# Optimization experiments

Measured on AMD Instinct MI355X. Metric: run time of the kernel, lower is better.

Reference implementation:

```python
import jax, jax.numpy as jnp
import numpy as np

B, K, HH, WW = 512, 256, 16, 16   # batch, channels (K//2 of init K=512), latent H, W
KH = 128                          # GRU hidden size
F = 16                            # future_window_lin


def gru_forward(seq, h0, W_ih, W_hh, b_ih, b_hh):
    # seq: (B,T,K) batch_first, h0: (B,KH). PyTorch GRU gate order: r, z, n.
    gx = jnp.einsum('btk,gk->btg', seq, W_ih) + b_ih  # (B,T,3*KH)

    def step(h, gx_t):
        gh = h @ W_hh.T + b_hh
        xr, xz, xn = jnp.split(gx_t, 3, axis=-1)
        hr, hz, hn = jnp.split(gh, 3, axis=-1)
        r = jax.nn.sigmoid(xr + hr)
        z = jax.nn.sigmoid(xz + hz)
        n = jnp.tanh(xn + r * hn)
        h_new = (1.0 - z) * n + z * h
        return h_new, h_new

    hT, outs = jax.lax.scan(step, h0, jnp.swapaxes(gx, 0, 1))  # outs: (T,B,KH)
    return jnp.swapaxes(outs, 0, 1), hT


def setup_inputs() -> dict:
    key = jax.random.key(0)
    ks = jax.random.split(key, 9)
    s = 0.05
    return {
        'z_q_x_st': jax.random.normal(ks[0], (B, K, HH, WW), jnp.float32),
        'z_e_x': jax.random.normal(ks[1], (B, K, HH, WW), jnp.float32),
        'z_q_x': jax.random.normal(ks[2], (B, K, HH, WW), jnp.float32),
        'hidden': jnp.zeros((1, B, KH), jnp.float32),
        'W_ih': jax.random.normal(ks[3], (3 * KH, K), jnp.float32) * s,
        'W_hh': jax.random.normal(ks[4], (3 * KH, KH), jnp.float32) * s,
        'b_ih': jnp.zeros((3 * KH,), jnp.float32),
        'b_hh': jnp.zeros((3 * KH,), jnp.float32),
        'Wk_w': jax.random.normal(ks[5], (F, K, KH), jnp.float32) * s,
        'Wk_b': jnp.zeros((F, K), jnp.float32),
        'p_sample': 100,
    }


def reference(z_q_x_st, z_e_x, z_q_x, hidden, W_ih, W_hh, b_ih, b_hh, Wk_w, Wk_b, p_sample):
    batch, k, h, w = z_e_x.shape
    f = Wk_w.shape[0]
    # (B,K,H,W) -> (B,H*W,K); row = idx//W, col = idx%W is just the row-major flat index
    z_flat = jnp.transpose(z_q_x_st, (0, 2, 3, 1)).reshape(batch, h * w, k)
    # encoded samples at flat positions p_sample+1 .. p_sample+F  -> (F,B,K)
    encoded = jnp.swapaxes(z_flat[:, p_sample + 1: p_sample + 1 + f, :], 0, 1)
    # GRU over the causal prefix; c_t = output at step p_sample (the last one)
    seq = z_flat[:, : p_sample + 1, :]
    out, _ = gru_forward(seq, hidden[0], W_ih, W_hh, b_ih, b_hh)
    c_t = out[:, -1, :]  # (B,KH)
    # per-step linear heads, batched: (F,B,K)
    pred = jnp.einsum('fkh,bh->fbk', Wk_w, c_t) + Wk_b[:, None, :]
    # totals[i] = encoded[i] @ pred[i].T  -> (F,B,B)
    totals = jnp.einsum('fbk,fck->fbc', encoded, pred)
    lsm = jax.nn.log_softmax(totals, axis=2)
    diag_sum = jnp.sum(jnp.diagonal(lsm, axis1=1, axis2=2))
    nce = -diag_sum / (batch * f)
    # 'correct' only reflects the last loop iteration in the torch code
    last = totals[-1]
    sm = jax.nn.softmax(last, axis=1)       # softmax over dim=1, then argmax over dim=0
    preds_idx = jnp.argmax(sm, axis=0)
    correct = jnp.sum(preds_idx == jnp.arange(batch))
    accuracy = correct.astype(jnp.float32) / batch
    return accuracy, nce, z_e_x, z_q_x
```

## Files before the change

kernel.cpp:

```cpp
#include <hip/hip_runtime.h>
#include <math.h>

#define NB_B   512
#define NK     256
#define NKH    128
#define NG3    384
#define NT     101
#define NF     16
#define NPASS  (512ull*256*256)

#define OFF_GX   0ull
#define N_GX     (512ull*101*384)
#define OFF_CT   (OFF_GX + N_GX)
#define OFF_ENC  (OFF_CT + 512ull*128)
#define OFF_PRED (OFF_ENC + 16ull*512*256)
#define OFF_TOT  (OFF_PRED + 16ull*512*256)
#define OFF_LSE  (OFF_TOT + 16ull*512*512)
#define OFF_DML  (OFF_LSE + 8192ull)
#define OFF_WT   (OFF_DML + 8192ull)
#define OFF_WKT  (OFF_WT + 384ull*256)
#define OFF_CNT  (OFF_WKT + 16ull*128*256)

__global__ __launch_bounds__(256) void k_transpose(
    const float* __restrict__ W_ih, const float* __restrict__ Wk_w,
    float* __restrict__ Wt, float* __restrict__ Wkt, int* __restrict__ cnt) {
  int idx = blockIdx.x * 256 + threadIdx.x;
  if (idx == 0) *cnt = 0;
  if (idx < 384 * 256) {
    int g = idx % 384, k = idx / 384;
    Wt[idx] = W_ih[g * 256 + k];
  }
  if (idx < 16 * 128 * 256) {
    int k = idx & 255, h = (idx >> 8) & 127, f = idx >> 15;
    Wkt[idx] = Wk_w[(f * 256 + k) * 128 + h];
  }
}

__global__ __launch_bounds__(768) void k_gx(
    const float* __restrict__ zq, const float* __restrict__ Wt,
    const float* __restrict__ b_ih, const float* __restrict__ b_hh,
    float* __restrict__ gx) {
  __shared__ float Xs[32][104];
  __shared__ float Ws[32 * 384];
  int b = blockIdx.x;
  int tid = threadIdx.x;
  int q = tid % 96;
  int tt = tid / 96;
  int g0 = q * 4;
  int t0 = tt * 13;
  int lane = tid & 63, wid = tid >> 6;
  float acc[4][13];
#pragma unroll
  for (int i = 0; i < 4; i++)
#pragma unroll
    for (int j = 0; j < 13; j++) acc[i][j] = 0.f;
  const float* zb = zq + (size_t)b * 65536;
  for (int kc = 0; kc < 8; kc++) {
    __syncthreads();
    for (int k = wid; k < 32; k += 12) {
      int kk = kc * 32 + k;
      Xs[k][lane] = zb[kk * 256 + lane];
      int t1 = 64 + lane;
      if (t1 < 104) Xs[k][t1] = (t1 < 101) ? zb[kk * 256 + t1] : 0.f;
    }
    {
      const float4* wsrc = (const float4*)(Wt + (size_t)kc * 32 * 384);
      float4* wdst = (float4*)Ws;
      for (int i = tid; i < 3072; i += 768) wdst[i] = wsrc[i];
    }
    __syncthreads();
    for (int k = 0; k < 32; k++) {
      float4 w = *(const float4*)&Ws[k * 384 + g0];
      const float* xr = &Xs[k][t0];
#pragma unroll
      for (int j = 0; j < 13; j++) {
        float x = xr[j];
        acc[0][j] += w.x * x;
        acc[1][j] += w.y * x;
        acc[2][j] += w.z * x;
        acc[3][j] += w.w * x;
      }
    }
  }
  float4 bias = *(const float4*)&b_ih[g0];
  if (g0 + 3 < 256) {
    bias.x += b_hh[g0 + 0]; bias.y += b_hh[g0 + 1];
    bias.z += b_hh[g0 + 2]; bias.w += b_hh[g0 + 3];
  }
#pragma unroll
  for (int j = 0; j < 13; j++) {
    int t = t0 + j;
    if (t < 101) {
      float4 v = make_float4(acc[0][j] + bias.x, acc[1][j] + bias.y,
                             acc[2][j] + bias.z, acc[3][j] + bias.w);
      *(float4*)&gx[(size_t)t * (512 * 384) + b * 384 + g0] = v;
    }
  }
}

__global__ __launch_bounds__(1024, 4) void k_scan(
    const float* __restrict__ gx, const float* __restrict__ W_hh,
    const float* __restrict__ b_hh, const float* __restrict__ hidden,
    float* __restrict__ ct,
    const float* __restrict__ src0, const float* __restrict__ src1,
    float2* __restrict__ d0, float2* __restrict__ d1) {
  __shared__ float hs[2][128];
  __shared__ float ghp[2][2][384];
  int tid = threadIdx.x;
  int b0 = blockIdx.x * 2;
  bool copy_role = (tid >= 768);

  int kh = tid / 384;
  int g = tid % 384;
  int lane = tid & 63;
  float w[64];
  float cxr = 0.f, cxz = 0.f, cxn = 0.f, nxr = 0.f, nxz = 0.f, nxn = 0.f;
  float bhn = 0.f;
  const float2* S0 = (const float2*)src0;
  const float2* S1 = (const float2*)src1;
  int c = tid - 768;
  size_t sbase = (size_t)blockIdx.x * 65536;
  int p = 0;

  if (!copy_role) {
    const float* wp = W_hh + g * 128 + kh * 64;
#pragma unroll
    for (int i = 0; i < 16; i++) {
      float4 v = *(const float4*)(wp + 4 * i);
      w[4 * i + 0] = v.x; w[4 * i + 1] = v.y;
      w[4 * i + 2] = v.z; w[4 * i + 3] = v.w;
    }
    if (tid < 256) {
      int r = tid >> 7, k = tid & 127;
      hs[r][k] = hidden[(b0 + r) * 128 + k];
      bhn = b_hh[256 + k];
      const float* gxb = gx + (b0 + r) * 384;
      cxr = gxb[k]; cxz = gxb[128 + k]; cxn = gxb[256 + k];
    }
  }
  __syncthreads();

  for (int t = 0; t < 101; t++) {
    if (!copy_role) {
      float hr0 = hs[0][kh * 64 + lane];
      float hr1 = hs[1][kh * 64 + lane];
      float a0 = 0.f, a1 = 0.f;
#pragma unroll
      for (int j = 0; j < 64; j++) {
        float h0 = __int_as_float(__builtin_amdgcn_readlane(__float_as_int(hr0), j));
        float h1 = __int_as_float(__builtin_amdgcn_readlane(__float_as_int(hr1), j));
        a0 = fmaf(w[j], h0, a0);
        a1 = fmaf(w[j], h1, a1);
      }
      ghp[0][kh][g] = a0;
      ghp[1][kh][g] = a1;
      if (tid < 256 && t < 100) {
        int r = tid >> 7, k = tid & 127;
        const float* gxb = gx + (size_t)(t + 1) * (512 * 384) + (b0 + r) * 384;
        nxr = gxb[k]; nxz = gxb[128 + k]; nxn = gxb[256 + k];
      }
    } else {
#pragma unroll
      for (int uu = 0; uu < 5; uu++) {
        int u = p + uu;
        size_t idx = sbase + (size_t)(u >> 1) * 256 + c;
        if (u & 1) d1[idx] = S1[idx];
        else       d0[idx] = S0[idx];
      }
      p += 5;
    }
    __syncthreads();
    if (!copy_role && tid < 256) {
      int r = tid >> 7, k = tid & 127;
      float hrr = ghp[r][0][k] + ghp[r][1][k];
      float hzz = ghp[r][0][128 + k] + ghp[r][1][128 + k];
      float hnn = ghp[r][0][256 + k] + ghp[r][1][256 + k] + bhn;
      float rr = 1.f / (1.f + __expf(-(cxr + hrr)));
      float zz = 1.f / (1.f + __expf(-(cxz + hzz)));
      float nn = tanhf(cxn + rr * hnn);
      hs[r][k] = (1.f - zz) * nn + zz * hs[r][k];
      cxr = nxr; cxz = nxz; cxn = nxn;
    }
    __syncthreads();
  }

  if (!copy_role && tid < 256) {
    int r = tid >> 7, k = tid & 127;
    ct[(b0 + r) * 128 + k] = hs[r][k];
  }
  if (copy_role) {
    for (; p < 512; p++) {
      size_t idx = sbase + (size_t)(p >> 1) * 256 + c;
      if (p & 1) d1[idx] = S1[idx];
      else       d0[idx] = S0[idx];
    }
  }
}

__global__ __launch_bounds__(256) void k_enc(const float* __restrict__ zq,
                                             float* __restrict__ enc) {
  __shared__ float tile[256][17];
  int b = blockIdx.x, tid = threadIdx.x;
  const float* zb = zq + (size_t)b * 65536;
  for (int pass = 0; pass < 16; pass++) {
    int idx = pass * 256 + tid;
    int k = idx >> 4, f = idx & 15;
    tile[k][f] = zb[k * 256 + 101 + f];
  }
  __syncthreads();
  for (int f = 0; f < 16; f++)
    enc[(size_t)f * 131072 + b * 256 + tid] = tile[tid][f];
}

__global__ __launch_bounds__(256) void k_pred(
    const float* __restrict__ Wkt, const float* __restrict__ Wk_b,
    const float* __restrict__ ct, float* __restrict__ pred) {
  __shared__ float cts[32][128];
  int f = blockIdx.x, c0 = blockIdx.y * 32;
  int tid = threadIdx.x;
  for (int pass = 0; pass < 16; pass++) {
    int idx = pass * 256 + tid;
    int cc = idx >> 7, h = idx & 127;
    cts[cc][h] = ct[(c0 + cc) * 128 + h];
  }
  __syncthreads();
  float acc[32];
#pragma unroll
  for (int i = 0; i < 32; i++) acc[i] = 0.f;
  const float* wb = Wkt + (size_t)f * 32768 + tid;
  for (int h = 0; h < 128; h += 4) {
    float w0 = wb[(h + 0) * 256], w1 = wb[(h + 1) * 256];
    float w2 = wb[(h + 2) * 256], w3 = wb[(h + 3) * 256];
#pragma unroll
    for (int cc = 0; cc < 32; cc++) {
      float4 cv = *(const float4*)&cts[cc][h];
      acc[cc] += w0 * cv.x + w1 * cv.y + w2 * cv.z + w3 * cv.w;
    }
  }
  float bias = Wk_b[f * 256 + tid];
#pragma unroll
  for (int cc = 0; cc < 32; cc++)
    pred[((size_t)f * 512 + c0 + cc) * 256 + tid] = acc[cc] + bias;
}

__global__ __launch_bounds__(256) void k_totals(
    const float* __restrict__ enc, const float* __restrict__ pred,
    float* __restrict__ tot) {
  __shared__ float As[32][68];
  __shared__ float Bs[32][68];
  int f = blockIdx.z, b0 = blockIdx.y * 64, c0 = blockIdx.x * 64;
  int tid = threadIdx.x;
  int tx = tid & 15, ty = tid >> 4;
  float acc[4][4];
#pragma unroll
  for (int i = 0; i < 4; i++)
#pragma unroll
    for (int j = 0; j < 4; j++) acc[i][j] = 0.f;
  const float* Ab = enc + (size_t)f * 131072;
  const float* Bb = pred + (size_t)f * 131072;
  int lr = tid >> 3;
  int lc = (tid & 7) * 4;
  for (int kc = 0; kc < 8; kc++) {
    int k0 = kc * 32;
    __syncthreads();
    float4 av0 = *(const float4*)&Ab[(b0 + lr) * 256 + k0 + lc];
    float4 av1 = *(const float4*)&Ab[(b0 + 32 + lr) * 256 + k0 + lc];
    float4 bv0 = *(const float4*)&Bb[(c0 + lr) * 256 + k0 + lc];
    float4 bv1 = *(const float4*)&Bb[(c0 + 32 + lr) * 256 + k0 + lc];
    As[lc + 0][lr] = av0.x; As[lc + 1][lr] = av0.y;
    As[lc + 2][lr] = av0.z; As[lc + 3][lr] = av0.w;
    As[lc + 0][lr + 32] = av1.x; As[lc + 1][lr + 32] = av1.y;
    As[lc + 2][lr + 32] = av1.z; As[lc + 3][lr + 32] = av1.w;
    Bs[lc + 0][lr] = bv0.x; Bs[lc + 1][lr] = bv0.y;
    Bs[lc + 2][lr] = bv0.z; Bs[lc + 3][lr] = bv0.w;
    Bs[lc + 0][lr + 32] = bv1.x; Bs[lc + 1][lr + 32] = bv1.y;
    Bs[lc + 2][lr + 32] = bv1.z; Bs[lc + 3][lr + 32] = bv1.w;
    __syncthreads();
#pragma unroll
    for (int kk = 0; kk < 32; kk++) {
      float4 a = *(const float4*)&As[kk][ty * 4];
      float4 bq = *(const float4*)&Bs[kk][tx * 4];
      acc[0][0] += a.x * bq.x; acc[0][1] += a.x * bq.y;
      acc[0][2] += a.x * bq.z; acc[0][3] += a.x * bq.w;
      acc[1][0] += a.y * bq.x; acc[1][1] += a.y * bq.y;
      acc[1][2] += a.y * bq.z; acc[1][3] += a.y * bq.w;
      acc[2][0] += a.z * bq.x; acc[2][1] += a.z * bq.y;
      acc[2][2] += a.z * bq.z; acc[2][3] += a.z * bq.w;
      acc[3][0] += a.w * bq.x; acc[3][1] += a.w * bq.y;
      acc[3][2] += a.w * bq.z; acc[3][3] += a.w * bq.w;
    }
  }
#pragma unroll
  for (int i = 0; i < 4; i++) {
    float4 v = make_float4(acc[i][0], acc[i][1], acc[i][2], acc[i][3]);
    *(float4*)&tot[(size_t)f * 262144 + (b0 + ty * 4 + i) * 512 + c0 + tx * 4] = v;
  }
}

__global__ __launch_bounds__(64) void k_lse(const float* __restrict__ tot,
                                            float* __restrict__ lse,
                                            float* __restrict__ dml) {
  int row = blockIdx.x;
  int b = row & 511;
  int lane = threadIdx.x;
  const float* tr = tot + (size_t)row * 512;
  float v[8];
  float mx = -1e30f;
#pragma unroll
  for (int i = 0; i < 8; i++) { v[i] = tr[i * 64 + lane]; mx = fmaxf(mx, v[i]); }
#pragma unroll
  for (int s = 32; s > 0; s >>= 1) mx = fmaxf(mx, __shfl_xor(mx, s));
  float sum = 0.f;
#pragma unroll
  for (int i = 0; i < 8; i++) sum += __expf(v[i] - mx);
#pragma unroll
  for (int s = 32; s > 0; s >>= 1) sum += __shfl_xor(sum, s);
  if (lane == 0) {
    float l = __logf(sum) + mx;
    lse[row] = l;
    dml[row] = tr[b] - l;
  }
}

__global__ __launch_bounds__(64) void k_acc(const float* __restrict__ tot,
                                            const float* __restrict__ lse,
                                            int* __restrict__ cnt) {
  int c = blockIdx.x;
  int lane = threadIdx.x;
  const float* t15 = tot + (size_t)15 * 262144;
  const float* l15 = lse + 15 * 512;
  float best = -1e30f;
  int bi = 1 << 30;
  for (int b = lane; b < 512; b += 64) {
    float v = t15[(size_t)b * 512 + c] - l15[b];
    if (v > best) { best = v; bi = b; }
  }
  for (int s = 32; s > 0; s >>= 1) {
    float ov = __shfl_xor(best, s);
    int oi = __shfl_xor(bi, s);
    if (ov > best || (ov == best && oi < bi)) { best = ov; bi = oi; }
  }
  if (lane == 0 && bi == c) atomicAdd(cnt, 1);
}

__global__ __launch_bounds__(256) void k_fin(const float* __restrict__ dml,
                                             const int* __restrict__ cnt,
                                             float* __restrict__ out) {
  __shared__ float red[256];
  int tid = threadIdx.x;
  float s = 0.f;
  for (int i = tid; i < 8192; i += 256) s += dml[i];
  red[tid] = s;
  __syncthreads();
  for (int st = 128; st > 0; st >>= 1) {
    if (tid < st) red[tid] += red[tid + st];
    __syncthreads();
  }
  if (tid == 0) {
    out[1] = -red[0] / 8192.f;
    out[0] = (float)(*cnt) / 512.f;
  }
}

extern "C" void kernel_launch(void* const* d_in, const int* in_sizes, int n_in,
                              void* d_out, int out_size, void* d_ws, size_t ws_size,
                              hipStream_t stream) {
  const float* zq   = (const float*)d_in[0];
  const float* ze   = (const float*)d_in[1];
  const float* zqx  = (const float*)d_in[2];
  const float* hid  = (const float*)d_in[3];
  const float* W_ih = (const float*)d_in[4];
  const float* W_hh = (const float*)d_in[5];
  const float* b_ih = (const float*)d_in[6];
  const float* b_hh = (const float*)d_in[7];
  const float* Wk_w = (const float*)d_in[8];
  const float* Wk_b = (const float*)d_in[9];
  float* out = (float*)d_out;
  float* ws  = (float*)d_ws;

  k_transpose<<<2048, 256, 0, stream>>>(W_ih, Wk_w, ws + OFF_WT, ws + OFF_WKT,
                                        (int*)(ws + OFF_CNT));
  k_gx<<<512, 768, 0, stream>>>(zq, ws + OFF_WT, b_ih, b_hh, ws + OFF_GX);
  k_scan<<<256, 1024, 0, stream>>>(ws + OFF_GX, W_hh, b_hh, hid, ws + OFF_CT,
                                   ze, zqx,
                                   (float2*)(out + 2), (float2*)(out + 2 + NPASS));
  k_enc<<<512, 256, 0, stream>>>(zq, ws + OFF_ENC);
  k_pred<<<dim3(16, 16), 256, 0, stream>>>(ws + OFF_WKT, Wk_b, ws + OFF_CT, ws + OFF_PRED);
  k_totals<<<dim3(8, 8, 16), 256, 0, stream>>>(ws + OFF_ENC, ws + OFF_PRED, ws + OFF_TOT);
  k_lse<<<8192, 64, 0, stream>>>(ws + OFF_TOT, ws + OFF_LSE, ws + OFF_DML);
  k_acc<<<512, 64, 0, stream>>>(ws + OFF_TOT, ws + OFF_LSE, (int*)(ws + OFF_CNT));
  k_fin<<<1, 256, 0, stream>>>(ws + OFF_DML, (const int*)(ws + OFF_CNT), out);
}
```

Before: 912.5 us.

## Widen gx GEMM register tile and pin scan W_hh weights in vector registers

The gx projection kernel now runs 384 threads per block, and each thread computes 8 gates by 13 timesteps instead of 4 by 13. This doubles register-level reuse of each shared-memory X load and halves the thread count. In the GRU scan, the 64 recurrent weights per thread are held as 16 float4 vectors, and an empty asm barrier at each step forces them to stay resident in VGPRs rather than be spilled or reloaded. The dot product is written out by hand with readlane broadcasts. The risks are higher register pressure in k_gx and constrained compiler scheduling in the scan.

```diff
diff --git a/kernel.cpp b/kernel.cpp
--- a/kernel.cpp
+++ b/kernel.cpp
@@ -21,6 +21,8 @@
 #define OFF_WKT  (OFF_WT + 384ull*256)
 #define OFF_CNT  (OFF_WKT + 16ull*128*256)
 
+typedef float f4v __attribute__((ext_vector_type(4)));
+
 __global__ __launch_bounds__(256) void k_transpose(
     const float* __restrict__ W_ih, const float* __restrict__ Wk_w,
     float* __restrict__ Wt, float* __restrict__ Wkt, int* __restrict__ cnt) {
@@ -36,7 +38,7 @@
   }
 }
 
-__global__ __launch_bounds__(768) void k_gx(
+__global__ __launch_bounds__(384, 2) void k_gx(
     const float* __restrict__ zq, const float* __restrict__ Wt,
     const float* __restrict__ b_ih, const float* __restrict__ b_hh,
     float* __restrict__ gx) {
@@ -44,20 +46,20 @@
   __shared__ float Ws[32 * 384];
   int b = blockIdx.x;
   int tid = threadIdx.x;
-  int q = tid % 96;
-  int tt = tid / 96;
-  int g0 = q * 4;
+  int q = tid % 48;
+  int tt = tid / 48;
+  int g0 = q * 8;
   int t0 = tt * 13;
   int lane = tid & 63, wid = tid >> 6;
-  float acc[4][13];
-#pragma unroll
-  for (int i = 0; i < 4; i++)
+  float acc[8][13];
+#pragma unroll
+  for (int i = 0; i < 8; i++)
 #pragma unroll
     for (int j = 0; j < 13; j++) acc[i][j] = 0.f;
   const float* zb = zq + (size_t)b * 65536;
   for (int kc = 0; kc < 8; kc++) {
     __syncthreads();
-    for (int k = wid; k < 32; k += 12) {
+    for (int k = wid; k < 32; k += 6) {
       int kk = kc * 32 + k;
       Xs[k][lane] = zb[kk * 256 + lane];
       int t1 = 64 + lane;
@@ -66,37 +68,60 @@
     {
       const float4* wsrc = (const float4*)(Wt + (size_t)kc * 32 * 384);
       float4* wdst = (float4*)Ws;
-      for (int i = tid; i < 3072; i += 768) wdst[i] = wsrc[i];
+      for (int i = tid; i < 3072; i += 384) wdst[i] = wsrc[i];
     }
     __syncthreads();
     for (int k = 0; k < 32; k++) {
-      float4 w = *(const float4*)&Ws[k * 384 + g0];
+      float4 wa = *(const float4*)&Ws[k * 384 + g0];
+      float4 wb = *(const float4*)&Ws[k * 384 + g0 + 4];
       const float* xr = &Xs[k][t0];
 #pragma unroll
       for (int j = 0; j < 13; j++) {
         float x = xr[j];
-        acc[0][j] += w.x * x;
-        acc[1][j] += w.y * x;
-        acc[2][j] += w.z * x;
-        acc[3][j] += w.w * x;
+        acc[0][j] += wa.x * x;
+        acc[1][j] += wa.y * x;
+        acc[2][j] += wa.z * x;
+        acc[3][j] += wa.w * x;
+        acc[4][j] += wb.x * x;
+        acc[5][j] += wb.y * x;
+        acc[6][j] += wb.z * x;
+        acc[7][j] += wb.w * x;
       }
     }
   }
-  float4 bias = *(const float4*)&b_ih[g0];
-  if (g0 + 3 < 256) {
-    bias.x += b_hh[g0 + 0]; bias.y += b_hh[g0 + 1];
-    bias.z += b_hh[g0 + 2]; bias.w += b_hh[g0 + 3];
+  float4 ba = *(const float4*)&b_ih[g0];
+  float4 bb = *(const float4*)&b_ih[g0 + 4];
+  if (g0 < 256) {
+    ba.x += b_hh[g0 + 0]; ba.y += b_hh[g0 + 1];
+    ba.z += b_hh[g0 + 2]; ba.w += b_hh[g0 + 3];
+    bb.x += b_hh[g0 + 4]; bb.y += b_hh[g0 + 5];
+    bb.z += b_hh[g0 + 6]; bb.w += b_hh[g0 + 7];
   }
 #pragma unroll
   for (int j = 0; j < 13; j++) {
     int t = t0 + j;
     if (t < 101) {
-      float4 v = make_float4(acc[0][j] + bias.x, acc[1][j] + bias.y,
-                             acc[2][j] + bias.z, acc[3][j] + bias.w);
-      *(float4*)&gx[(size_t)t * (512 * 384) + b * 384 + g0] = v;
-    }
-  }
-}
+      float* gp = &gx[(size_t)t * (512 * 384) + b * 384 + g0];
+      *(float4*)gp = make_float4(acc[0][j] + ba.x, acc[1][j] + ba.y,
+                                 acc[2][j] + ba.z, acc[3][j] + ba.w);
+      *(float4*)(gp + 4) = make_float4(acc[4][j] + bb.x, acc[5][j] + bb.y,
+                                       acc[6][j] + bb.z, acc[7][j] + bb.w);
+    }
+  }
+}
+
+#define RL(x, J) __int_as_float(__builtin_amdgcn_readlane(__float_as_int(x), (J)))
+#define DOT4(W, J)                                                   \
+  do {                                                               \
+    a0 = fmaf(W.x, RL(hr0, (J) + 0), a0);                            \
+    a1 = fmaf(W.x, RL(hr1, (J) + 0), a1);                            \
+    a0 = fmaf(W.y, RL(hr0, (J) + 1), a0);                            \
+    a1 = fmaf(W.y, RL(hr1, (J) + 1), a1);                            \
+    a0 = fmaf(W.z, RL(hr0, (J) + 2), a0);                            \
+    a1 = fmaf(W.z, RL(hr1, (J) + 2), a1);                            \
+    a0 = fmaf(W.w, RL(hr0, (J) + 3), a0);                            \
+    a1 = fmaf(W.w, RL(hr1, (J) + 3), a1);                            \
+  } while (0)
 
 __global__ __launch_bounds__(1024, 4) void k_scan(
     const float* __restrict__ gx, const float* __restrict__ W_hh,
@@ -113,7 +138,7 @@
   int kh = tid / 384;
   int g = tid % 384;
   int lane = tid & 63;
-  float w[64];
+  f4v w0, w1, w2, w3, w4, w5, w6, w7, w8, w9, wA, wB, wC, wD, wE, wF;
   float cxr = 0.f, cxz = 0.f, cxn = 0.f, nxr = 0.f, nxz = 0.f, nxn = 0.f;
   float bhn = 0.f;
   const float2* S0 = (const float2*)src0;
@@ -123,13 +148,11 @@
   int p = 0;
 
   if (!copy_role) {
-    const float* wp = W_hh + g * 128 + kh * 64;
-#pragma unroll
-    for (int i = 0; i < 16; i++) {
-      float4 v = *(const float4*)(wp + 4 * i);
-      w[4 * i + 0] = v.x; w[4 * i + 1] = v.y;
-      w[4 * i + 2] = v.z; w[4 * i + 3] = v.w;
-    }
+    const f4v* wp = (const f4v*)(W_hh + g * 128 + kh * 64);
+    w0 = wp[0];  w1 = wp[1];  w2 = wp[2];  w3 = wp[3];
+    w4 = wp[4];  w5 = wp[5];  w6 = wp[6];  w7 = wp[7];
+    w8 = wp[8];  w9 = wp[9];  wA = wp[10]; wB = wp[11];
+    wC = wp[12]; wD = wp[13]; wE = wp[14]; wF = wp[15];
     if (tid < 256) {
       int r = tid >> 7, k = tid & 127;
       hs[r][k] = hidden[(b0 + r) * 128 + k];
@@ -142,16 +165,17 @@
 
   for (int t = 0; t < 101; t++) {
     if (!copy_role) {
+      asm volatile("" : "+v"(w0), "+v"(w1), "+v"(w2), "+v"(w3),
+                        "+v"(w4), "+v"(w5), "+v"(w6), "+v"(w7),
+                        "+v"(w8), "+v"(w9), "+v"(wA), "+v"(wB),
+                        "+v"(wC), "+v"(wD), "+v"(wE), "+v"(wF));
       float hr0 = hs[0][kh * 64 + lane];
       float hr1 = hs[1][kh * 64 + lane];
       float a0 = 0.f, a1 = 0.f;
-#pragma unroll
-      for (int j = 0; j < 64; j++) {
-        float h0 = __int_as_float(__builtin_amdgcn_readlane(__float_as_int(hr0), j));
-        float h1 = __int_as_float(__builtin_amdgcn_readlane(__float_as_int(hr1), j));
-        a0 = fmaf(w[j], h0, a0);
-        a1 = fmaf(w[j], h1, a1);
-      }
+      DOT4(w0, 0);  DOT4(w1, 4);  DOT4(w2, 8);  DOT4(w3, 12);
+      DOT4(w4, 16); DOT4(w5, 20); DOT4(w6, 24); DOT4(w7, 28);
+      DOT4(w8, 32); DOT4(w9, 36); DOT4(wA, 40); DOT4(wB, 44);
+      DOT4(wC, 48); DOT4(wD, 52); DOT4(wE, 56); DOT4(wF, 60);
       ghp[0][kh][g] = a0;
       ghp[1][kh][g] = a1;
       if (tid < 256 && t < 100) {
@@ -380,7 +404,7 @@
 
   k_transpose<<<2048, 256, 0, stream>>>(W_ih, Wk_w, ws + OFF_WT, ws + OFF_WKT,
                                         (int*)(ws + OFF_CNT));
-  k_gx<<<512, 768, 0, stream>>>(zq, ws + OFF_WT, b_ih, b_hh, ws + OFF_GX);
+  k_gx<<<512, 384, 0, stream>>>(zq, ws + OFF_WT, b_ih, b_hh, ws + OFF_GX);
   k_scan<<<256, 1024, 0, stream>>>(ws + OFF_GX, W_hh, b_hh, hid, ws + OFF_CT,
                                    ze, zqx,
                                    (float2*)(out + 2), (float2*)(out + 2 + NPASS));
```

New measurement: 962.5 us. 5.5% more time.

## Broadcast GRU hidden state via global memory and scalar loads instead of readlane

Applied to the files above, without the earlier changes.

The recurrent scan no longer keeps the hidden state in shared memory and broadcasts it with per-lane readlane calls. Each step's hidden state is now written to a global history buffer, which reuses the encoder/pred workspace region. The matvec threads then read it back with s_load_dwordx16 scalar loads in four chunks, which removes the 128 readlane instructions per step. The cost is a global-memory round trip and four serialized scalar-load waits on the critical path of every step. It also relies on vector stores becoming visible to scalar loads after the barrier.

```diff
diff --git a/kernel.cpp b/kernel.cpp
--- a/kernel.cpp
+++ b/kernel.cpp
@@ -20,6 +20,10 @@
 #define OFF_WT   (OFF_DML + 8192ull)
 #define OFF_WKT  (OFF_WT + 384ull*256)
 #define OFF_CNT  (OFF_WKT + 16ull*128*256)
+#define OFF_HG   OFF_ENC
+
+typedef float f4v __attribute__((ext_vector_type(4)));
+typedef int  si16 __attribute__((ext_vector_type(16)));
 
 __global__ __launch_bounds__(256) void k_transpose(
     const float* __restrict__ W_ih, const float* __restrict__ Wk_w,
@@ -98,41 +102,55 @@
   }
 }
 
+#define SCHUNK(C, OFF0, OFF1)                                            \
+  {                                                                      \
+    si16 ha_, hb_;                                                       \
+    asm volatile("s_load_dwordx16 %0, %2, " OFF0 "\n\t"                  \
+                 "s_load_dwordx16 %1, %2, " OFF1 "\n\t"                  \
+                 "s_waitcnt lgkmcnt(0)"                                  \
+                 : "=s"(ha_), "=s"(hb_)                                  \
+                 : "s"(ua)                                               \
+                 : "memory");                                            \
+    _Pragma("unroll")                                                    \
+    for (int jj = 0; jj < 16; jj++) {                                    \
+      float wv = wq[(C) * 4 + (jj >> 2)][jj & 3];                        \
+      a0 = fmaf(wv, __int_as_float(ha_[jj]), a0);                        \
+      a1 = fmaf(wv, __int_as_float(hb_[jj]), a1);                        \
+    }                                                                    \
+  }
+
 __global__ __launch_bounds__(1024, 4) void k_scan(
     const float* __restrict__ gx, const float* __restrict__ W_hh,
     const float* __restrict__ b_hh, const float* __restrict__ hidden,
     float* __restrict__ ct,
     const float* __restrict__ src0, const float* __restrict__ src1,
-    float2* __restrict__ d0, float2* __restrict__ d1) {
-  __shared__ float hs[2][128];
+    float2* __restrict__ d0, float2* __restrict__ d1,
+    float* __restrict__ hgl) {
   __shared__ float ghp[2][2][384];
   int tid = threadIdx.x;
-  int b0 = blockIdx.x * 2;
+  int blk = blockIdx.x;
+  int b0 = blk * 2;
   bool copy_role = (tid >= 768);
 
-  int kh = tid / 384;
+  int khu = __builtin_amdgcn_readfirstlane(tid / 384);
   int g = tid % 384;
-  int lane = tid & 63;
-  float w[64];
+  f4v wq[16];
   float cxr = 0.f, cxz = 0.f, cxn = 0.f, nxr = 0.f, nxz = 0.f, nxn = 0.f;
-  float bhn = 0.f;
+  float bhn = 0.f, h_own = 0.f;
   const float2* S0 = (const float2*)src0;
   const float2* S1 = (const float2*)src1;
   int c = tid - 768;
-  size_t sbase = (size_t)blockIdx.x * 65536;
+  size_t sbase = (size_t)blk * 65536;
   int p = 0;
 
   if (!copy_role) {
-    const float* wp = W_hh + g * 128 + kh * 64;
-#pragma unroll
-    for (int i = 0; i < 16; i++) {
-      float4 v = *(const float4*)(wp + 4 * i);
-      w[4 * i + 0] = v.x; w[4 * i + 1] = v.y;
-      w[4 * i + 2] = v.z; w[4 * i + 3] = v.w;
-    }
+    const f4v* wp = (const f4v*)(W_hh + g * 128 + khu * 64);
+#pragma unroll
+    for (int i = 0; i < 16; i++) wq[i] = wp[i];
     if (tid < 256) {
       int r = tid >> 7, k = tid & 127;
-      hs[r][k] = hidden[(b0 + r) * 128 + k];
+      h_own = hidden[(b0 + r) * 128 + k];
+      hgl[blk * 256 + r * 128 + k] = h_own;
       bhn = b_hh[256 + k];
       const float* gxb = gx + (b0 + r) * 384;
       cxr = gxb[k]; cxz = gxb[128 + k]; cxn = gxb[256 + k];
@@ -142,18 +160,19 @@
 
   for (int t = 0; t < 101; t++) {
     if (!copy_role) {
-      float hr0 = hs[0][kh * 64 + lane];
-      float hr1 = hs[1][kh * 64 + lane];
+      const float* hp = hgl + (size_t)t * 65536 + (size_t)blk * 256 + khu * 64;
+      unsigned int alo = __builtin_amdgcn_readfirstlane(
+          (unsigned int)(unsigned long long)hp);
+      unsigned int ahi = __builtin_amdgcn_readfirstlane(
+          (unsigned int)((unsigned long long)hp >> 32));
+      unsigned long long ua = ((unsigned long long)ahi << 32) | alo;
       float a0 = 0.f, a1 = 0.f;
-#pragma unroll
-      for (int j = 0; j < 64; j++) {
-        float h0 = __int_as_float(__builtin_amdgcn_readlane(__float_as_int(hr0), j));
-        float h1 = __int_as_float(__builtin_amdgcn_readlane(__float_as_int(hr1), j));
-        a0 = fmaf(w[j], h0, a0);
-        a1 = fmaf(w[j], h1, a1);
-      }
-      ghp[0][kh][g] = a0;
-      ghp[1][kh][g] = a1;
+      SCHUNK(0, "0x0",  "0x200")
+      SCHUNK(1, "0x40", "0x240")
+      SCHUNK(2, "0x80", "0x280")
+      SCHUNK(3, "0xC0", "0x2C0")
+      ghp[0][khu][g] = a0;
+      ghp[1][khu][g] = a1;
       if (tid < 256 && t < 100) {
         int r = tid >> 7, k = tid & 127;
         const float* gxb = gx + (size_t)(t + 1) * (512 * 384) + (b0 + r) * 384;
@@ -178,7 +197,8 @@
       float rr = 1.f / (1.f + __expf(-(cxr + hrr)));
       float zz = 1.f / (1.f + __expf(-(cxz + hzz)));
       float nn = tanhf(cxn + rr * hnn);
-      hs[r][k] = (1.f - zz) * nn + zz * hs[r][k];
+      h_own = (1.f - zz) * nn + zz * h_own;
+      hgl[(size_t)(t + 1) * 65536 + blk * 256 + r * 128 + k] = h_own;
       cxr = nxr; cxz = nxz; cxn = nxn;
     }
     __syncthreads();
@@ -186,7 +206,7 @@
 
   if (!copy_role && tid < 256) {
     int r = tid >> 7, k = tid & 127;
-    ct[(b0 + r) * 128 + k] = hs[r][k];
+    ct[(b0 + r) * 128 + k] = h_own;
   }
   if (copy_role) {
     for (; p < 512; p++) {
@@ -383,7 +403,8 @@
   k_gx<<<512, 768, 0, stream>>>(zq, ws + OFF_WT, b_ih, b_hh, ws + OFF_GX);
   k_scan<<<256, 1024, 0, stream>>>(ws + OFF_GX, W_hh, b_hh, hid, ws + OFF_CT,
                                    ze, zqx,
-                                   (float2*)(out + 2), (float2*)(out + 2 + NPASS));
+                                   (float2*)(out + 2), (float2*)(out + 2 + NPASS),
+                                   ws + OFF_HG);
   k_enc<<<512, 256, 0, stream>>>(zq, ws + OFF_ENC);
   k_pred<<<dim3(16, 16), 256, 0, stream>>>(ws + OFF_WKT, Wk_b, ws + OFF_CT, ws + OFF_PRED);
   k_totals<<<dim3(8, 8, 16), 256, 0, stream>>>(ws + OFF_ENC, ws + OFF_PRED, ws + OFF_TOT);
```

Result: slower. 979.3 us (+7.3%).
